# Optimization experiments

Measured on AMD Instinct MI355X. Metric: run time of the kernel, lower is better.

Reference implementation:

```python
import jax, jax.numpy as jnp
import numpy as np


def setup_inputs() -> dict:
    key = jax.random.key(0)
    k1, k2, k3 = jax.random.split(key, 3)
    B, S, D_IN, D_OUT = 2, 2048, 4096, 4096
    x = jax.random.normal(k1, (B, S, D_IN), dtype=jnp.float32)
    # int8 quantized weight (stored as int32 container, values in int8 range)
    weight = jax.random.randint(k2, (D_OUT, D_IN), 0, 127, dtype=jnp.int32)
    weight_scaler = jax.random.uniform(k3, (D_OUT,), dtype=jnp.float32)
    return {"x": x, "weight": weight, "weight_scaler": weight_scaler}


def reference(x, weight, weight_scaler):
    # Dequantize per-output-channel: w_fp = int8_weight * scaler[:, None]
    w = weight.astype(jnp.float32) * weight_scaler[:, None]  # [O, I]
    # F.linear: x @ w.T
    return jnp.einsum("bsi,oi->bso", x, w)
```

## Files before the change

kernel.cpp:

```cpp
#include <hip/hip_runtime.h>

typedef int i32x4 __attribute__((ext_vector_type(4)));

#define AS1 __attribute__((address_space(1)))
#define AS3 __attribute__((address_space(3)))

__global__ __launch_bounds__(256) void quant_kernel(
    const float4* __restrict__ x, const int4* __restrict__ w,
    signed char* __restrict__ xq, signed char* __restrict__ wq,
    float* __restrict__ sx, int M, int Kq) {
  const int tid = threadIdx.x;
  if ((int)blockIdx.x < M) {
    const int r = blockIdx.x;
    float4 v[4];
    #pragma unroll
    for (int j = 0; j < 4; ++j) v[j] = x[(size_t)r * 1024 + tid * 4 + j];
    float m = 0.f;
    #pragma unroll
    for (int j = 0; j < 4; ++j)
      m = fmaxf(m, fmaxf(fmaxf(fabsf(v[j].x), fabsf(v[j].y)),
                         fmaxf(fabsf(v[j].z), fabsf(v[j].w))));
    #pragma unroll
    for (int off = 1; off < 64; off <<= 1) m = fmaxf(m, __shfl_xor(m, off));
    __shared__ float wmax[4];
    if ((tid & 63) == 0) wmax[tid >> 6] = m;
    __syncthreads();
    m = fmaxf(fmaxf(wmax[0], wmax[1]), fmaxf(wmax[2], wmax[3]));
    const float inv = (m > 0.f) ? 127.0f / m : 0.f;
    if (tid == 0) sx[r] = m * (1.0f / 127.0f);
    signed char q[16];
    #pragma unroll
    for (int j = 0; j < 4; ++j) {
      q[j * 4 + 0] = (signed char)__float2int_rn(v[j].x * inv);
      q[j * 4 + 1] = (signed char)__float2int_rn(v[j].y * inv);
      q[j * 4 + 2] = (signed char)__float2int_rn(v[j].z * inv);
      q[j * 4 + 3] = (signed char)__float2int_rn(v[j].w * inv);
    }
    ((int4*)xq)[(size_t)r * 256 + tid] = *(const int4*)q;
  } else {
    const int b = blockIdx.x - M;
    int4 v[4];
    #pragma unroll
    for (int j = 0; j < 4; ++j) v[j] = w[(size_t)b * 1024 + tid * 4 + j];
    signed char q[16];
    #pragma unroll
    for (int j = 0; j < 4; ++j) {
      q[j * 4 + 0] = (signed char)v[j].x; q[j * 4 + 1] = (signed char)v[j].y;
      q[j * 4 + 2] = (signed char)v[j].z; q[j * 4 + 3] = (signed char)v[j].w;
    }
    ((int4*)wq)[(size_t)b * 256 + tid] = *(const int4*)q;
  }
}

__global__ __launch_bounds__(256) void gemm_i8_kernel(
    const signed char* __restrict__ A,
    const signed char* __restrict__ B,
    const float* __restrict__ sx,
    const float* __restrict__ scaler,
    float* __restrict__ C,
    int M, int N, int K)
{
  __shared__ signed char sA[128 * 128];
  __shared__ signed char sB[128 * 128];

  const int tid  = threadIdx.x;
  const int wave = tid >> 6;
  const int lane = tid & 63;
  const int bm = blockIdx.y << 7;
  const int bn = blockIdx.x << 7;

  const int wm = (wave >> 1) << 6;
  const int wn = (wave & 1) << 6;
  const int l15  = lane & 15;
  const int quad = lane >> 4;

  const int l8 = lane >> 3;
  const int kg = (lane & 7) ^ l8;
  const signed char* ga = A + (size_t)(bm + wave * 8 + l8) * K + kg * 16;
  const signed char* gb = B + (size_t)(bn + wave * 8 + l8) * K + kg * 16;
  const size_t cstep = (size_t)32 * K;

  signed char* lA = &sA[wave * 1024];
  signed char* lB = &sB[wave * 1024];

  i32x4 acc[4][4] = {};

  for (int k0 = 0; k0 < K; k0 += 128) {
    #pragma unroll
    for (int c = 0; c < 4; ++c) {
      __builtin_amdgcn_global_load_lds((AS1 void*)(ga + k0 + c * cstep), (AS3 void*)(lA + c * 4096), 16, 0, 0);
      __builtin_amdgcn_global_load_lds((AS1 void*)(gb + k0 + c * cstep), (AS3 void*)(lB + c * 4096), 16, 0, 0);
    }
    __syncthreads();

    #pragma unroll
    for (int s = 0; s < 2; ++s) {
      i32x4 av[4], bv[4];
      const int pk = ((s << 2) | quad) ^ (l15 & 7);
      #pragma unroll
      for (int mi = 0; mi < 4; ++mi)
        av[mi] = *(const i32x4*)&sA[(wm + mi * 16 + l15) * 128 + pk * 16];
      #pragma unroll
      for (int ni = 0; ni < 4; ++ni)
        bv[ni] = *(const i32x4*)&sB[(wn + ni * 16 + l15) * 128 + pk * 16];

      #pragma unroll
      for (int mi = 0; mi < 4; ++mi)
        #pragma unroll
        for (int ni = 0; ni < 4; ++ni)
          acc[mi][ni] = __builtin_amdgcn_mfma_i32_16x16x64_i8(av[mi], bv[ni], acc[mi][ni], 0, 0, 0);
    }
    __syncthreads();
  }

  #pragma unroll
  for (int mi = 0; mi < 4; ++mi) {
    const int gm0 = bm + wm + mi * 16 + quad * 4;
    float sr[4];
    #pragma unroll
    for (int r = 0; r < 4; ++r) sr[r] = sx[gm0 + r];
    #pragma unroll
    for (int ni = 0; ni < 4; ++ni) {
      const int gn = bn + wn + ni * 16 + l15;
      const float sc = scaler[gn];
      #pragma unroll
      for (int r = 0; r < 4; ++r)
        C[(size_t)(gm0 + r) * N + gn] = (float)acc[mi][ni][r] * sr[r] * sc;
    }
  }
}

extern "C" void kernel_launch(void* const* d_in, const int* in_sizes, int n_in,
                              void* d_out, int out_size, void* d_ws, size_t ws_size,
                              hipStream_t stream) {
  const float* x  = (const float*)d_in[0];
  const int*   w  = (const int*)d_in[1];
  const float* sc = (const float*)d_in[2];
  float* out = (float*)d_out;

  const int N = in_sizes[2];
  const int K = in_sizes[1] / N;
  const int M = in_sizes[0] / K;

  signed char* Aq = (signed char*)d_ws;
  signed char* Bq = Aq + (size_t)M * K;
  float* sx = (float*)(Bq + (size_t)N * K);

  const int wBlocks = (N * K) / (256 * 16);
  quant_kernel<<<M + wBlocks, 256, 0, stream>>>(
      (const float4*)x, (const int4*)w, Aq, Bq, sx, M, K / 16);

  dim3 grid(N / 128, M / 128);
  gemm_i8_kernel<<<grid, 256, 0, stream>>>(Aq, Bq, sx, sc, out, M, N, K);
}
```

Baseline: 244.5 us.

## Use 256x256 tiles with 8 waves and a 4-stage LDS pipeline

The int8 GEMM moves from 128x128 tiles with 4 waves to 256x256 tiles with 8 waves, each wave computing 128x64. It streams K in steps of 64 through a 4-buffer LDS ring with prefetch two steps ahead, using explicit vmcnt waits, split barriers and s_setprio around the MFMA bursts. The aim is to overlap global-to-LDS loads with MFMA work and to raise data reuse per tile. In exchange it uses more LDS and more accumulator registers, and the grid drops to 256 blocks, which may underfill the GPU.

Measured after the change: 252.1 us. 3.1% more time.

```diff
diff --git a/kernel.cpp b/kernel.cpp
--- a/kernel.cpp
+++ b/kernel.cpp
@@ -52,7 +52,7 @@
   }
 }
 
-__global__ __launch_bounds__(256) void gemm_i8_kernel(
+__global__ __launch_bounds__(512, 2) void gemm_i8_kernel(
     const signed char* __restrict__ A,
     const signed char* __restrict__ B,
     const float* __restrict__ sx,
@@ -60,61 +60,94 @@
     float* __restrict__ C,
     int M, int N, int K)
 {
-  __shared__ signed char sA[128 * 128];
-  __shared__ signed char sB[128 * 128];
+  __shared__ signed char sA[4][256 * 64];
+  __shared__ signed char sB[4][256 * 64];
 
   const int tid  = threadIdx.x;
   const int wave = tid >> 6;
   const int lane = tid & 63;
-  const int bm = blockIdx.y << 7;
-  const int bn = blockIdx.x << 7;
+  const int bm = blockIdx.y << 8;
+  const int bn = blockIdx.x << 8;
 
-  const int wm = (wave >> 1) << 6;
-  const int wn = (wave & 1) << 6;
+  const int wm = (wave >> 2) << 7;
+  const int wn = (wave & 3) << 6;
   const int l15  = lane & 15;
   const int quad = lane >> 4;
 
-  const int l8 = lane >> 3;
-  const int kg = (lane & 7) ^ l8;
-  const signed char* ga = A + (size_t)(bm + wave * 8 + l8) * K + kg * 16;
-  const signed char* gb = B + (size_t)(bn + wave * 8 + l8) * K + kg * 16;
-  const size_t cstep = (size_t)32 * K;
+  const int srow = tid >> 2;
+  const int kg = (tid & 3) ^ ((srow >> 1) & 3);
+  const signed char* ga = A + (size_t)(bm + srow) * K + kg * 16;
+  const signed char* gb = B + (size_t)(bn + srow) * K + kg * 16;
+  const size_t rstep = (size_t)128 * K;
+  const int ldst = tid * 16;
 
-  signed char* lA = &sA[wave * 1024];
-  signed char* lB = &sB[wave * 1024];
+  const int pk   = (quad ^ ((l15 >> 1) & 3)) << 4;
+  const int aoff = (wm + l15) * 64 + pk;
+  const int boff = (wn + l15) * 64 + pk;
 
-  i32x4 acc[4][4] = {};
+  i32x4 acc[8][4] = {};
 
-  for (int k0 = 0; k0 < K; k0 += 128) {
+#define STAGE_A(tt) do { const int sb_ = (tt) & 3;                           \
+    __builtin_amdgcn_global_load_lds((AS1 void*)(ga + (size_t)(tt) * 64),    \
+                                     (AS3 void*)(&sA[sb_][ldst]), 16, 0, 0); \
+    __builtin_amdgcn_global_load_lds((AS1 void*)(ga + (size_t)(tt) * 64 + rstep), \
+                                     (AS3 void*)(&sA[sb_][8192 + ldst]), 16, 0, 0); } while (0)
+#define STAGE_B(tt) do { const int sb_ = (tt) & 3;                           \
+    __builtin_amdgcn_global_load_lds((AS1 void*)(gb + (size_t)(tt) * 64),    \
+                                     (AS3 void*)(&sB[sb_][ldst]), 16, 0, 0); \
+    __builtin_amdgcn_global_load_lds((AS1 void*)(gb + (size_t)(tt) * 64 + rstep), \
+                                     (AS3 void*)(&sB[sb_][8192 + ldst]), 16, 0, 0); } while (0)
+
+  const int nt = K >> 6;
+
+  STAGE_A(0); STAGE_B(0); STAGE_A(1); STAGE_B(1);
+  asm volatile("s_waitcnt vmcnt(4)" ::: "memory");
+  __builtin_amdgcn_s_barrier();
+  __builtin_amdgcn_sched_barrier(0);
+
+  for (int t = 0; t < nt; ++t) {
+    const signed char* la = sA[t & 3];
+    const signed char* lb = sB[t & 3];
+    const bool st = (t < nt - 2);
+    i32x4 av[4], bv[4];
+
+    if (st) STAGE_A(t + 2);
     #pragma unroll
-    for (int c = 0; c < 4; ++c) {
-      __builtin_amdgcn_global_load_lds((AS1 void*)(ga + k0 + c * cstep), (AS3 void*)(lA + c * 4096), 16, 0, 0);
-      __builtin_amdgcn_global_load_lds((AS1 void*)(gb + k0 + c * cstep), (AS3 void*)(lB + c * 4096), 16, 0, 0);
-    }
-    __syncthreads();
-
+    for (int ni = 0; ni < 4; ++ni) bv[ni] = *(const i32x4*)&lb[boff + ni * 1024];
     #pragma unroll
-    for (int s = 0; s < 2; ++s) {
-      i32x4 av[4], bv[4];
-      const int pk = ((s << 2) | quad) ^ (l15 & 7);
-      #pragma unroll
-      for (int mi = 0; mi < 4; ++mi)
-        av[mi] = *(const i32x4*)&sA[(wm + mi * 16 + l15) * 128 + pk * 16];
+    for (int mi = 0; mi < 4; ++mi) av[mi] = *(const i32x4*)&la[aoff + mi * 1024];
+    __builtin_amdgcn_s_barrier();
+    __builtin_amdgcn_s_setprio(1);
+    #pragma unroll
+    for (int mi = 0; mi < 4; ++mi)
       #pragma unroll
       for (int ni = 0; ni < 4; ++ni)
-        bv[ni] = *(const i32x4*)&sB[(wn + ni * 16 + l15) * 128 + pk * 16];
+        acc[mi][ni] = __builtin_amdgcn_mfma_i32_16x16x64_i8(av[mi], bv[ni], acc[mi][ni], 0, 0, 0);
+    __builtin_amdgcn_s_setprio(0);
+    __builtin_amdgcn_s_barrier();
 
+    if (st) STAGE_B(t + 2);
+    #pragma unroll
+    for (int mi = 0; mi < 4; ++mi) av[mi] = *(const i32x4*)&la[aoff + (mi + 4) * 1024];
+    __builtin_amdgcn_s_barrier();
+    __builtin_amdgcn_s_setprio(1);
+    #pragma unroll
+    for (int mi = 0; mi < 4; ++mi)
       #pragma unroll
-      for (int mi = 0; mi < 4; ++mi)
-        #pragma unroll
-        for (int ni = 0; ni < 4; ++ni)
-          acc[mi][ni] = __builtin_amdgcn_mfma_i32_16x16x64_i8(av[mi], bv[ni], acc[mi][ni], 0, 0, 0);
-    }
-    __syncthreads();
+      for (int ni = 0; ni < 4; ++ni)
+        acc[mi + 4][ni] = __builtin_amdgcn_mfma_i32_16x16x64_i8(av[mi], bv[ni], acc[mi + 4][ni], 0, 0, 0);
+    __builtin_amdgcn_s_setprio(0);
+
+    if (st)                 asm volatile("s_waitcnt vmcnt(4)" ::: "memory");
+    else if (t == nt - 2)   asm volatile("s_waitcnt vmcnt(0)" ::: "memory");
+    __builtin_amdgcn_s_barrier();
+    __builtin_amdgcn_sched_barrier(0);
   }
+#undef STAGE_A
+#undef STAGE_B
 
   #pragma unroll
-  for (int mi = 0; mi < 4; ++mi) {
+  for (int mi = 0; mi < 8; ++mi) {
     const int gm0 = bm + wm + mi * 16 + quad * 4;
     float sr[4];
     #pragma unroll
@@ -150,6 +183,6 @@
   quant_kernel<<<M + wBlocks, 256, 0, stream>>>(
       (const float4*)x, (const int4*)w, Aq, Bq, sx, M, K / 16);
 
-  dim3 grid(N / 128, M / 128);
-  gemm_i8_kernel<<<grid, 256, 0, stream>>>(Aq, Bq, sx, sc, out, M, N, K);
+  dim3 grid(N / 256, M / 256);
+  gemm_i8_kernel<<<grid, 512, 0, stream>>>(Aq, Bq, sx, sc, out, M, N, K);
 }
```
